# Optimization experiments

Measured on AMD Instinct MI355X. Metric: run time of the kernel, lower is better.

## Reference

```python
import jax, jax.numpy as jnp
import numpy as np

B, I, H = 4096, 2048, 2048


def setup_inputs() -> dict:
    key = jax.random.key(0)
    k1, k2, k3, k4, k5 = jax.random.split(key, 5)
    return {
        "x": jax.random.normal(k1, (B, I), dtype=jnp.float32),
        "coefficients": jax.random.normal(k2, (I, H), dtype=jnp.float32) * 0.1,
        "amplitude_an": jax.random.normal(k3, (1, I, H), dtype=jnp.float32) * 0.1,
        "amplitude_bn": jax.random.normal(k4, (1, I, H), dtype=jnp.float32) * 0.1,
        "bias": jax.random.normal(k5, (1, I), dtype=jnp.float32),
    }


def reference(x, coefficients, amplitude_an, amplitude_bn, bias):
    # phase[b,h] = x[b,:] @ coefficients[:,h]  (same matmul done per-sample in torch loop)
    phase = x @ coefficients  # [B, H]
    num_harmonics = coefficients.shape[1]
    # sum over harmonics of an[i,h]*cos(phase[b,h]) + bn[i,h]*sin(phase[b,h])
    gain = (
        jnp.einsum("bh,ih->bi", jnp.cos(phase), amplitude_an[0])
        + jnp.einsum("bh,ih->bi", jnp.sin(phase), amplitude_bn[0])
        + num_harmonics * bias  # bias added per-harmonic before the sum over H
    )
    return gain  # [B, I]
```

## Files before the change

kernel.cpp:

```cpp
#include <hip/hip_runtime.h>
#include <hip/hip_bf16.h>

#define B_DIM 4096
#define I_DIM 2048
#define H_DIM 2048

typedef unsigned char u8;
typedef unsigned short u16;
typedef unsigned int u32;
typedef __attribute__((ext_vector_type(4))) float f32x4;
typedef __attribute__((ext_vector_type(4))) int i32x4;
typedef __attribute__((ext_vector_type(8))) int i32x8;

#define SBAR __builtin_amdgcn_sched_barrier(0)

__device__ __forceinline__ void gload_lds16(const void* g, void* l) {
  __builtin_amdgcn_global_load_lds(
      (const __attribute__((address_space(1))) void*)g,
      (__attribute__((address_space(3))) void*)l, 16, 0, 0);
}

__device__ __forceinline__ u32 f2fp4(float v, float inv_scale) {
  const float a = fabsf(v) * inv_scale;
  u32 m = (u32)(a > 0.25f) + (u32)(a > 0.75f) + (u32)(a > 1.25f) +
          (u32)(a > 1.75f) + (u32)(a > 2.5f) + (u32)(a > 3.5f) + (u32)(a > 5.0f);
  return ((__float_as_uint(v) >> 31) << 3) | m;
}

__global__ void prep_all(const float* __restrict__ x, const float* __restrict__ coeff,
                         const float* __restrict__ an, const float* __restrict__ bn,
                         u16* __restrict__ xf4, u16* __restrict__ ct4,
                         u32* __restrict__ ab4) {
  if (blockIdx.x < 4096) {
    __shared__ float tile[32][33];
    const int h0 = (blockIdx.x & 63) * 32;
    const int i0 = (blockIdx.x >> 6) * 32;
    const int tid = threadIdx.x;
    const int tx = tid & 31;
    const int ty = tid >> 5;
    for (int r = ty; r < 32; r += 8)
      tile[r][tx] = coeff[(long)(i0 + r) * H_DIM + (h0 + tx)];
    __syncthreads();
    const int hl = tid >> 3;
    const int q = (tid & 7) * 4;
    u32 w = f2fp4(tile[q + 0][hl], 8.f) | (f2fp4(tile[q + 1][hl], 8.f) << 4) |
            (f2fp4(tile[q + 2][hl], 8.f) << 8) | (f2fp4(tile[q + 3][hl], 8.f) << 12);
    ct4[(long)(h0 + hl) * (I_DIM / 4) + ((i0 + q) >> 2)] = (u16)w;
    return;
  }
  const long NX4 = (long)B_DIM * I_DIM / 4;
  const long NA4 = (long)I_DIM * H_DIM / 4;
  const long total = NX4 + NA4;
  const long stride = (long)1024 * blockDim.x;
  for (long t = (long)(blockIdx.x - 4096) * blockDim.x + threadIdx.x; t < total;
       t += stride) {
    if (t < NX4) {
      float4 v = *(const float4*)(x + t * 4);
      u32 b0 = f2fp4(v.x, 1.f) | (f2fp4(v.y, 1.f) << 4);
      u32 b1 = f2fp4(v.z, 1.f) | (f2fp4(v.w, 1.f) << 4);
      xf4[t] = (u16)(b0 | (b1 << 8));
    } else {
      long p = (t - NX4) * 4;
      float4 va = *(const float4*)(an + p);
      float4 vb = *(const float4*)(bn + p);
      u32 b0 = f2fp4(va.x, 8.f) | (f2fp4(vb.x, 8.f) << 4);
      u32 b1 = f2fp4(va.y, 8.f) | (f2fp4(vb.y, 8.f) << 4);
      u32 b2 = f2fp4(va.z, 8.f) | (f2fp4(vb.z, 8.f) << 4);
      u32 b3 = f2fp4(va.w, 8.f) | (f2fp4(vb.w, 8.f) << 4);
      ab4[p >> 2] = b0 | (b1 << 8) | (b2 << 16) | (b3 << 24);
    }
  }
}

__device__ __forceinline__ void stage_tile(const char* Ab, const char* Bb, long kbyte,
                                           long lda, long ldb, char* AsB, char* BsB,
                                           int tid) {
#pragma unroll
  for (int i = 0; i < 4; ++i) {
    const int o = i * 4096 + tid * 16;
    const int row = o >> 7;
    const int ls = ((((o >> 4) & 7) ^ (row & 7)) << 4);
    gload_lds16(Ab + (long)row * lda + kbyte + ls, AsB + o);
  }
#pragma unroll
  for (int i = 0; i < 4; ++i) {
    const int o = i * 4096 + tid * 16;
    const int row = o >> 7;
    const int ls = ((((o >> 4) & 7) ^ (row & 7)) << 4);
    gload_lds16(Bb + (long)row * ldb + kbyte + ls, BsB + o);
  }
}

__device__ __forceinline__ i32x4 frag_ld16(const char* S, int row, int slot) {
  return *(const i32x4*)(S + row * 128 + ((slot ^ (row & 7)) << 4));
}

template <int SA, int SB>
__device__ __forceinline__ void gemm_kloop_fp4(const char* __restrict__ A,
                                               const char* __restrict__ Bt,
                                               int rowA0, int colB0, long Kbytes,
                                               char* smem, f32x4 acc[4][4]) {
  const int tid = threadIdx.x;
  const int lane = tid & 63;
  const int wid = tid >> 6;
  const int wr = wid >> 1, wc = wid & 1;
  const long lda = Kbytes, ldb = Kbytes;
  const char* Ab = A + (long)rowA0 * lda;
  const char* Bb = Bt + (long)colB0 * ldb;
  const int arow = wr * 64 + (lane & 15);
  const int brow = wc * 64 + (lane & 15);
  const int g = lane >> 4;
  const int nt = (int)(Kbytes >> 7);
  char* AsB = smem;
  char* BsB = smem + 16384;

  stage_tile(Ab, Bb, 0, lda, ldb, AsB, BsB, tid);
  stage_tile(Ab, Bb, 128, lda, ldb, AsB + 32768, BsB + 32768, tid);

  for (int t = 0; t < nt; ++t) {
    const int cur = (t & 1) << 15;
    if (t < nt - 1) asm volatile("s_waitcnt vmcnt(8)" ::: "memory");
    else            asm volatile("s_waitcnt vmcnt(0)" ::: "memory");
    SBAR;
    __builtin_amdgcn_s_barrier();
    SBAR;

    i32x8 af[8], bfr[8];
#pragma unroll
    for (int s = 0; s < 2; ++s)
#pragma unroll
      for (int m = 0; m < 4; ++m) {
        *(i32x4*)&af[s * 4 + m]  = frag_ld16(AsB + cur, arow + m * 16, s * 4 + g);
        *(i32x4*)&bfr[s * 4 + m] = frag_ld16(BsB + cur, brow + m * 16, s * 4 + g);
      }
    asm volatile("s_waitcnt lgkmcnt(0)" ::: "memory");
    SBAR;
    __builtin_amdgcn_s_barrier();
    SBAR;

    if (t + 2 < nt)
      stage_tile(Ab, Bb, (long)(t + 2) * 128, lda, ldb, AsB + cur, BsB + cur, tid);

    __builtin_amdgcn_s_setprio(1);
#pragma unroll
    for (int s = 0; s < 2; ++s)
#pragma unroll
      for (int m = 0; m < 4; ++m)
#pragma unroll
        for (int n = 0; n < 4; ++n)
          acc[m][n] = __builtin_amdgcn_mfma_scale_f32_16x16x128_f8f6f4(
              af[s * 4 + m], bfr[s * 4 + n], acc[m][n], 4, 4, 0, SA, 0, SB);
    __builtin_amdgcn_s_setprio(0);
    SBAR;
  }
}

__device__ __forceinline__ void tile_xy(int& bx, int& by) {
  const int bid = blockIdx.x;
  const int xcd = bid & 7;
  const int loc = bid >> 3;
  const int cy = xcd >> 1;
  const int cx = xcd & 1;
  by = cy * 8 + (loc >> 3);
  bx = cx * 8 + (loc & 7);
}

__global__ __launch_bounds__(256) void gemm_phase(const char* __restrict__ xf4,
                                                  const char* __restrict__ ct4,
                                                  u8* __restrict__ cs4) {
  __shared__ __align__(16) char smem[65536];
  int bx, by;
  tile_xy(bx, by);
  const int rowA0 = by * 128;
  const int colB0 = bx * 128;
  f32x4 acc[4][4];
#pragma unroll
  for (int m = 0; m < 4; ++m)
#pragma unroll
    for (int n = 0; n < 4; ++n)
#pragma unroll
      for (int j = 0; j < 4; ++j) acc[m][n][j] = 0.0f;

  gemm_kloop_fp4<0x7F7F7F7F, 0x7C7C7C7C>(xf4, ct4, rowA0, colB0, I_DIM / 2, smem, acc);

  const int lane = threadIdx.x & 63;
  const int wid = threadIdx.x >> 6;
  const int wr = wid >> 1, wc = wid & 1;
#pragma unroll
  for (int m = 0; m < 4; ++m) {
#pragma unroll
    for (int n = 0; n < 4; ++n) {
      const int col = colB0 + wc * 64 + n * 16 + (lane & 15);
#pragma unroll
      for (int j = 0; j < 4; ++j) {
        const int row = rowA0 + wr * 64 + m * 16 + (lane >> 4) * 4 + j;
        const float p = acc[m][n][j];
        float sp, cp;
        __sincosf(p, &sp, &cp);
        const u32 b = f2fp4(cp, 4.f) | (f2fp4(sp, 4.f) << 4);
        cs4[(long)row * H_DIM + col] = (u8)b;
      }
    }
  }
}

__global__ __launch_bounds__(256) void gemm_gain(const char* __restrict__ cs4,
                                                 const char* __restrict__ ab4,
                                                 const float* __restrict__ bias,
                                                 float* __restrict__ out) {
  __shared__ __align__(16) char smem[65536];
  int bx, by;
  tile_xy(bx, by);
  const int rowA0 = by * 128;
  const int colB0 = bx * 128;
  f32x4 acc[4][4];
#pragma unroll
  for (int m = 0; m < 4; ++m)
#pragma unroll
    for (int n = 0; n < 4; ++n)
#pragma unroll
      for (int j = 0; j < 4; ++j) acc[m][n][j] = 0.0f;

  gemm_kloop_fp4<0x7D7D7D7D, 0x7C7C7C7C>(cs4, ab4, rowA0, colB0, H_DIM, smem, acc);

  const int lane = threadIdx.x & 63;
  const int wid = threadIdx.x >> 6;
  const int wr = wid >> 1, wc = wid & 1;
#pragma unroll
  for (int m = 0; m < 4; ++m) {
#pragma unroll
    for (int n = 0; n < 4; ++n) {
      const int col = colB0 + wc * 64 + n * 16 + (lane & 15);
      const float bv = 2048.0f * bias[col];
#pragma unroll
      for (int j = 0; j < 4; ++j) {
        const int row = rowA0 + wr * 64 + m * 16 + (lane >> 4) * 4 + j;
        out[(long)row * I_DIM + col] = acc[m][n][j] + bv;
      }
    }
  }
}

extern "C" void kernel_launch(void* const* d_in, const int* in_sizes, int n_in,
                              void* d_out, int out_size, void* d_ws, size_t ws_size,
                              hipStream_t stream) {
  const float* x     = (const float*)d_in[0];
  const float* coeff = (const float*)d_in[1];
  const float* an    = (const float*)d_in[2];
  const float* bn    = (const float*)d_in[3];
  const float* bias  = (const float*)d_in[4];
  float* out = (float*)d_out;

  char* ws = (char*)d_ws;
  char* xf4 = ws;
  char* ct4 = ws + (4L << 20);
  char* ab4 = ws + (8L << 20);
  u8*  cs4  = (u8*)(ws + (12L << 20));

  prep_all<<<5120, 256, 0, stream>>>(x, coeff, an, bn, (u16*)xf4, (u16*)ct4,
                                     (u32*)ab4);
  gemm_phase<<<512, 256, 0, stream>>>(xf4, ct4, cs4);
  gemm_gain<<<512, 256, 0, stream>>>((const char*)cs4, (const char*)ab4, bias, out);
}
```

Baseline: 65.96 us.

## Move amplitude quantization into phase GEMM and use 32x32 MFMA for gain GEMM

Quantizing the an/bn amplitudes to fp4 moves out of the prep kernel and into the tail of the phase GEMM kernel, where it can overlap with that kernel's compute-bound tiles. The prep kernel becomes smaller. The gain GEMM switches from 16x16x128 to 32x32x64 scaled MFMA tiles, which cuts fragment loads per MFMA and changes the accumulator layout and epilogue indexing. This adds memory traffic to the end of the phase kernel and raises per-wave register pressure from the larger accumulators.

```diff
diff --git a/kernel.cpp b/kernel.cpp
--- a/kernel.cpp
+++ b/kernel.cpp
@@ -9,6 +9,7 @@
 typedef unsigned short u16;
 typedef unsigned int u32;
 typedef __attribute__((ext_vector_type(4))) float f32x4;
+typedef __attribute__((ext_vector_type(16))) float f32x16;
 typedef __attribute__((ext_vector_type(4))) int i32x4;
 typedef __attribute__((ext_vector_type(8))) int i32x8;
 
@@ -27,10 +28,8 @@
   return ((__float_as_uint(v) >> 31) << 3) | m;
 }
 
-__global__ void prep_all(const float* __restrict__ x, const float* __restrict__ coeff,
-                         const float* __restrict__ an, const float* __restrict__ bn,
-                         u16* __restrict__ xf4, u16* __restrict__ ct4,
-                         u32* __restrict__ ab4) {
+__global__ void prep_xc(const float* __restrict__ x, const float* __restrict__ coeff,
+                        u16* __restrict__ xf4, u16* __restrict__ ct4) {
   if (blockIdx.x < 4096) {
     __shared__ float tile[32][33];
     const int h0 = (blockIdx.x & 63) * 32;
@@ -49,26 +48,13 @@
     return;
   }
   const long NX4 = (long)B_DIM * I_DIM / 4;
-  const long NA4 = (long)I_DIM * H_DIM / 4;
-  const long total = NX4 + NA4;
-  const long stride = (long)1024 * blockDim.x;
-  for (long t = (long)(blockIdx.x - 4096) * blockDim.x + threadIdx.x; t < total;
+  const long stride = (long)512 * blockDim.x;
+  for (long t = (long)(blockIdx.x - 4096) * blockDim.x + threadIdx.x; t < NX4;
        t += stride) {
-    if (t < NX4) {
-      float4 v = *(const float4*)(x + t * 4);
-      u32 b0 = f2fp4(v.x, 1.f) | (f2fp4(v.y, 1.f) << 4);
-      u32 b1 = f2fp4(v.z, 1.f) | (f2fp4(v.w, 1.f) << 4);
-      xf4[t] = (u16)(b0 | (b1 << 8));
-    } else {
-      long p = (t - NX4) * 4;
-      float4 va = *(const float4*)(an + p);
-      float4 vb = *(const float4*)(bn + p);
-      u32 b0 = f2fp4(va.x, 8.f) | (f2fp4(vb.x, 8.f) << 4);
-      u32 b1 = f2fp4(va.y, 8.f) | (f2fp4(vb.y, 8.f) << 4);
-      u32 b2 = f2fp4(va.z, 8.f) | (f2fp4(vb.z, 8.f) << 4);
-      u32 b3 = f2fp4(va.w, 8.f) | (f2fp4(vb.w, 8.f) << 4);
-      ab4[p >> 2] = b0 | (b1 << 8) | (b2 << 16) | (b3 << 24);
-    }
+    float4 v = *(const float4*)(x + t * 4);
+    u32 b0 = f2fp4(v.x, 1.f) | (f2fp4(v.y, 1.f) << 4);
+    u32 b1 = f2fp4(v.z, 1.f) | (f2fp4(v.w, 1.f) << 4);
+    xf4[t] = (u16)(b0 | (b1 << 8));
   }
 }
 
@@ -155,6 +141,66 @@
   }
 }
 
+template <int SA, int SB>
+__device__ __forceinline__ void gemm_kloop_fp4_32(const char* __restrict__ A,
+                                                  const char* __restrict__ Bt,
+                                                  int rowA0, int colB0, long Kbytes,
+                                                  char* smem, f32x16 acc[2][2]) {
+  const int tid = threadIdx.x;
+  const int lane = tid & 63;
+  const int wid = tid >> 6;
+  const int wr = wid >> 1, wc = wid & 1;
+  const long lda = Kbytes, ldb = Kbytes;
+  const char* Ab = A + (long)rowA0 * lda;
+  const char* Bb = Bt + (long)colB0 * ldb;
+  const int arow = wr * 64 + (lane & 31);
+  const int brow = wc * 64 + (lane & 31);
+  const int h = lane >> 5;
+  const int nt = (int)(Kbytes >> 7);
+  char* AsB = smem;
+  char* BsB = smem + 16384;
+
+  stage_tile(Ab, Bb, 0, lda, ldb, AsB, BsB, tid);
+  stage_tile(Ab, Bb, 128, lda, ldb, AsB + 32768, BsB + 32768, tid);
+
+  for (int t = 0; t < nt; ++t) {
+    const int cur = (t & 1) << 15;
+    if (t < nt - 1) asm volatile("s_waitcnt vmcnt(8)" ::: "memory");
+    else            asm volatile("s_waitcnt vmcnt(0)" ::: "memory");
+    SBAR;
+    __builtin_amdgcn_s_barrier();
+    SBAR;
+
+    i32x8 af[2][4], bfr[2][4];
+#pragma unroll
+    for (int m = 0; m < 2; ++m)
+#pragma unroll
+      for (int kb = 0; kb < 4; ++kb) {
+        *(i32x4*)&af[m][kb]  = frag_ld16(AsB + cur, arow + m * 32, 2 * kb + h);
+        *(i32x4*)&bfr[m][kb] = frag_ld16(BsB + cur, brow + m * 32, 2 * kb + h);
+      }
+    asm volatile("s_waitcnt lgkmcnt(0)" ::: "memory");
+    SBAR;
+    __builtin_amdgcn_s_barrier();
+    SBAR;
+
+    if (t + 2 < nt)
+      stage_tile(Ab, Bb, (long)(t + 2) * 128, lda, ldb, AsB + cur, BsB + cur, tid);
+
+    __builtin_amdgcn_s_setprio(1);
+#pragma unroll
+    for (int kb = 0; kb < 4; ++kb)
+#pragma unroll
+      for (int m = 0; m < 2; ++m)
+#pragma unroll
+        for (int n = 0; n < 2; ++n)
+          acc[m][n] = __builtin_amdgcn_mfma_scale_f32_32x32x64_f8f6f4(
+              af[m][kb], bfr[n][kb], acc[m][n], 4, 4, 0, SA, 0, SB);
+    __builtin_amdgcn_s_setprio(0);
+    SBAR;
+  }
+}
+
 __device__ __forceinline__ void tile_xy(int& bx, int& by) {
   const int bid = blockIdx.x;
   const int xcd = bid & 7;
@@ -167,7 +213,10 @@
 
 __global__ __launch_bounds__(256) void gemm_phase(const char* __restrict__ xf4,
                                                   const char* __restrict__ ct4,
-                                                  u8* __restrict__ cs4) {
+                                                  u8* __restrict__ cs4,
+                                                  const float* __restrict__ an,
+                                                  const float* __restrict__ bn,
+                                                  u32* __restrict__ ab4) {
   __shared__ __align__(16) char smem[65536];
   int bx, by;
   tile_xy(bx, by);
@@ -202,6 +251,19 @@
       }
     }
   }
+
+  const long NA4 = (long)I_DIM * H_DIM / 4;
+  const long stride = (long)512 * blockDim.x;
+  for (long t = (long)blockIdx.x * blockDim.x + threadIdx.x; t < NA4; t += stride) {
+    long p = t * 4;
+    float4 va = *(const float4*)(an + p);
+    float4 vb = *(const float4*)(bn + p);
+    u32 b0 = f2fp4(va.x, 8.f) | (f2fp4(vb.x, 8.f) << 4);
+    u32 b1 = f2fp4(va.y, 8.f) | (f2fp4(vb.y, 8.f) << 4);
+    u32 b2 = f2fp4(va.z, 8.f) | (f2fp4(vb.z, 8.f) << 4);
+    u32 b3 = f2fp4(va.w, 8.f) | (f2fp4(vb.w, 8.f) << 4);
+    ab4[t] = b0 | (b1 << 8) | (b2 << 16) | (b3 << 24);
+  }
 }
 
 __global__ __launch_bounds__(256) void gemm_gain(const char* __restrict__ cs4,
@@ -213,29 +275,30 @@
   tile_xy(bx, by);
   const int rowA0 = by * 128;
   const int colB0 = bx * 128;
-  f32x4 acc[4][4];
-#pragma unroll
-  for (int m = 0; m < 4; ++m)
-#pragma unroll
-    for (int n = 0; n < 4; ++n)
-#pragma unroll
-      for (int j = 0; j < 4; ++j) acc[m][n][j] = 0.0f;
-
-  gemm_kloop_fp4<0x7D7D7D7D, 0x7C7C7C7C>(cs4, ab4, rowA0, colB0, H_DIM, smem, acc);
+  f32x16 acc[2][2];
+#pragma unroll
+  for (int m = 0; m < 2; ++m)
+#pragma unroll
+    for (int n = 0; n < 2; ++n)
+#pragma unroll
+      for (int j = 0; j < 16; ++j) acc[m][n][j] = 0.0f;
+
+  gemm_kloop_fp4_32<0x7D7D7D7D, 0x7C7C7C7C>(cs4, ab4, rowA0, colB0, H_DIM, smem, acc);
 
   const int lane = threadIdx.x & 63;
   const int wid = threadIdx.x >> 6;
   const int wr = wid >> 1, wc = wid & 1;
 #pragma unroll
-  for (int m = 0; m < 4; ++m) {
-#pragma unroll
-    for (int n = 0; n < 4; ++n) {
-      const int col = colB0 + wc * 64 + n * 16 + (lane & 15);
+  for (int m = 0; m < 2; ++m) {
+#pragma unroll
+    for (int n = 0; n < 2; ++n) {
+      const int col = colB0 + wc * 64 + n * 32 + (lane & 31);
       const float bv = 2048.0f * bias[col];
 #pragma unroll
-      for (int j = 0; j < 4; ++j) {
-        const int row = rowA0 + wr * 64 + m * 16 + (lane >> 4) * 4 + j;
-        out[(long)row * I_DIM + col] = acc[m][n][j] + bv;
+      for (int reg = 0; reg < 16; ++reg) {
+        const int row = rowA0 + wr * 64 + m * 32 + (reg & 3) + 8 * (reg >> 2) +
+                        4 * (lane >> 5);
+        out[(long)row * I_DIM + col] = acc[m][n][reg] + bv;
       }
     }
   }
@@ -257,8 +320,7 @@
   char* ab4 = ws + (8L << 20);
   u8*  cs4  = (u8*)(ws + (12L << 20));
 
-  prep_all<<<5120, 256, 0, stream>>>(x, coeff, an, bn, (u16*)xf4, (u16*)ct4,
-                                     (u32*)ab4);
-  gemm_phase<<<512, 256, 0, stream>>>(xf4, ct4, cs4);
+  prep_xc<<<4608, 256, 0, stream>>>(x, coeff, (u16*)xf4, (u16*)ct4);
+  gemm_phase<<<512, 256, 0, stream>>>(xf4, ct4, cs4, an, bn, (u32*)ab4);
   gemm_gain<<<512, 256, 0, stream>>>((const char*)cs4, (const char*)ab4, bias, out);
 }
```

After: 67.29 us. 2.0% more time.
